# Optimization experiments

Hardware: AMD Instinct MI355X
Metric: run time of the kernel (lower is better)

Reference implementation:

```python
import jax, jax.numpy as jnp
import numpy as np

N = 50000      # nodes
E = 400000     # edges
D = 128        # embedding_depth
H = 4          # attention heads
DK = 32        # per-head dim (graph_message_depth / heads)
NR = 50        # num_radial
L = 2          # num_graph_convolutions
NG = 100       # graphs in batch
NT = 100       # atom type vocab
TE = 32        # atom_type_embedding_dims
OUT = 512      # bottleneck_dim
CUT = 6.0      # convolution_cutoff


def setup_inputs() -> dict:
    key = jax.random.key(0)
    ks = jax.random.split(key, 20)
    s = 0.05
    inp = {
        'pos': jax.random.normal(ks[0], (N, 3), jnp.float32) * 5.0,
        'atom_types': jax.random.randint(ks[1], (N,), 0, NT),
        'edge_index': jax.random.randint(ks[2], (2, E), 0, N),
        'batch': jnp.sort(jax.random.randint(ks[3], (N,), 0, NG)),
        'emb_table': jax.random.normal(ks[4], (NT, TE), jnp.float32) * s,
        'W_init': jax.random.normal(ks[5], (TE + 3, D), jnp.float32) * s,
        'b_init': jnp.zeros((D,), jnp.float32),
        'Wq': jax.random.normal(ks[6], (L, D, H * DK), jnp.float32) * s,
        'Wk': jax.random.normal(ks[7], (L, D, H * DK), jnp.float32) * s,
        'Wv': jax.random.normal(ks[8], (L, D, H * DK), jnp.float32) * s,
        'We': jax.random.normal(ks[9], (L, NR, H * DK), jnp.float32) * s,
        'Wo': jax.random.normal(ks[10], (L, H * DK, D), jnp.float32) * s,
        'Wm1': jax.random.normal(ks[11], (L, D, D), jnp.float32) * s,
        'bm1': jnp.zeros((L, D), jnp.float32),
        'Wm2': jax.random.normal(ks[12], (L, D, D), jnp.float32) * s,
        'bm2': jnp.zeros((L, D), jnp.float32),
        'ln_g': jnp.ones((L, D), jnp.float32),
        'ln_b': jnp.zeros((L, D), jnp.float32),
        'W_out': jax.random.normal(ks[13], (D, OUT), jnp.float32) * s,
        'b_out': jnp.zeros((OUT,), jnp.float32),
    }
    return inp


def _layernorm(x, g, b):
    m = jnp.mean(x, -1, keepdims=True)
    v = jnp.var(x, -1, keepdims=True)
    return (x - m) * jax.lax.rsqrt(v + 1e-5) * g + b


def _rbf(d):
    # Gaussian radial basis with smooth cosine cutoff envelope
    mus = jnp.linspace(0.0, CUT, NR)
    gamma = (NR / CUT) ** 2
    env = 0.5 * (jnp.cos(jnp.pi * jnp.minimum(d, CUT) / CUT) + 1.0)
    return jnp.exp(-gamma * (d[:, None] - mus[None, :]) ** 2) * env[:, None]


def _seg_softmax(logits, seg, n):
    # logits: [E, H], segmented softmax over incoming edges per node
    m = jax.ops.segment_max(logits, seg, num_segments=n)
    e = jnp.exp(logits - m[seg])
    s = jax.ops.segment_sum(e, seg, num_segments=n)
    return e / (s[seg] + 1e-9)


def _forward(pos, atom_types, edge_index, batch, emb_table, W_init, b_init,
             Wq, Wk, Wv, We, Wo, Wm1, bm1, Wm2, bm2, ln_g, ln_b, W_out, b_out):
    src, dst = edge_index[0], edge_index[1]
    # atom type embedding + concat positions -> init node features
    x0 = jnp.concatenate([emb_table[atom_types], pos], axis=-1)  # [N, TE+3]
    x = x0 @ W_init + b_init                                     # [N, D]
    # radial features per edge
    d = jnp.linalg.norm(pos[src] - pos[dst] + 1e-8, axis=-1)     # [E]
    rb = _rbf(d)                                                 # [E, NR]
    scale = 1.0 / jnp.sqrt(jnp.float32(DK))
    for l in range(L):
        qn, kn, vn = x @ Wq[l], x @ Wk[l], x @ Wv[l]             # [N, H*DK]
        q = qn[dst].reshape(E, H, DK)
        k = kn[src].reshape(E, H, DK)
        v = vn[src].reshape(E, H, DK)
        e = (rb @ We[l]).reshape(E, H, DK)
        logits = jnp.sum(q * (k + e), axis=-1) * scale           # [E, H]
        a = _seg_softmax(logits, dst, N)                         # [E, H]
        msg = jax.ops.segment_sum(a[..., None] * (v + e), dst, num_segments=N)
        x = x + msg.reshape(N, H * DK) @ Wo[l]
        # nodewise FC block with pre-norm and residual
        h = _layernorm(x, ln_g[l], ln_b[l])
        h = jax.nn.gelu(h @ Wm1[l] + bm1[l])
        x = x + h @ Wm2[l] + bm2[l]
    # sum graph aggregation, then output projection to bottleneck
    g = jax.ops.segment_sum(x, batch, num_segments=NG)           # [NG, D]
    return g @ W_out + b_out                                     # [NG, OUT]


def reference(pos, atom_types, edge_index, batch, emb_table, W_init, b_init,
              Wq, Wk, Wv, We, Wo, Wm1, bm1, Wm2, bm2, ln_g, ln_b, W_out, b_out):
    return _forward(pos, atom_types, edge_index, batch, emb_table, W_init, b_init,
                    Wq, Wk, Wv, We, Wo, Wm1, bm1, Wm2, bm2, ln_g, ln_b, W_out, b_out)
```

## Files before the change

kernel.cpp:

```cpp
#include <hip/hip_runtime.h>
#include <math.h>

#define NN 50000
#define NE 400000
#define DDIM 128
#define NHEAD 4
#define NRAD 50
#define NGRAPH 100
#define NTYPE 100
#define TEMB 32
#define DOUT 512
#define CUTF 6.0f
#define PI_F 3.14159265358979323846f

#define SCAN_N ((NN + 255) / 256)

typedef unsigned int uint;
typedef unsigned short ushort;
typedef __attribute__((ext_vector_type(8))) short short8;
typedef __attribute__((ext_vector_type(4))) float f32x4;


__device__ __forceinline__ float gelu_tanh(float v) {
  float u = 0.7978845608028654f * (v + 0.044715f * v * v * v);
  return 0.5f * v * (1.0f + tanhf(u));
}

__device__ __forceinline__ ushort f2bf(float f) {
  uint u = __float_as_uint(f);
  uint r = (u + 0x7fffu + ((u >> 16) & 1u)) >> 16;
  return (ushort)r;
}
__device__ __forceinline__ float bfl(uint u) { return __uint_as_float(u << 16); }
__device__ __forceinline__ float bfh(uint u) { return __uint_as_float(u & 0xffff0000u); }

__device__ __forceinline__ float red16(float v) {
  v += __int_as_float(__builtin_amdgcn_update_dpp(0, __float_as_int(v), 0xB1, 0xF, 0xF, true));
  v += __int_as_float(__builtin_amdgcn_update_dpp(0, __float_as_int(v), 0x4E, 0xF, 0xF, true));
  v += __int_as_float(__builtin_amdgcn_update_dpp(0, __float_as_int(v), 0x141, 0xF, 0xF, true));
  v += __int_as_float(__builtin_amdgcn_update_dpp(0, __float_as_int(v), 0x140, 0xF, 0xF, true));
  return v;
}
__device__ __forceinline__ float red8(float v) {
  v += __int_as_float(__builtin_amdgcn_update_dpp(0, __float_as_int(v), 0xB1, 0xF, 0xF, true));
  v += __int_as_float(__builtin_amdgcn_update_dpp(0, __float_as_int(v), 0x4E, 0xF, 0xF, true));
  v += __int_as_float(__builtin_amdgcn_update_dpp(0, __float_as_int(v), 0x141, 0xF, 0xF, true));
  return v;
}

__global__ void k_fill_f(float* p, float v, int n) {
  int i = blockIdx.x * blockDim.x + threadIdx.x;
  if (i < n) p[i] = v;
}
__global__ void k_fill_i(int* p, int v, int n) {
  int i = blockIdx.x * blockDim.x + threadIdx.x;
  if (i < n) p[i] = v;
}


__global__ void k_wconv(const float* __restrict__ Wq, const float* __restrict__ Wk,
                        const float* __restrict__ Wv, const float* __restrict__ Wo,
                        const float* __restrict__ Wm1, const float* __restrict__ Wm2,
                        ushort* __restrict__ Wtb) {
  int idx = blockIdx.x * 256 + threadIdx.x;
  int m = idx >> 14;
  int r = idx & 16383;
  int c = r >> 7, k = r & 127;
  int l = m / 6, fam = m % 6;
  const float* src = fam == 0 ? Wq : fam == 1 ? Wk : fam == 2 ? Wv
                   : fam == 3 ? Wo : fam == 4 ? Wm1 : Wm2;
  Wtb[idx] = f2bf(src[l * 16384 + k * 128 + c]);
}


__global__ void k_wewo(const float* __restrict__ We, const float* __restrict__ Wo,
                       ushort* __restrict__ WW) {
  int idx = blockIdx.x * 256 + threadIdx.x;
  int l = idx >> 15;
  int r = idx & 32767;
  int c = r >> 8, k = r & 255;
  float acc = 0.f;
  if (k < 200) {
    int j = k >> 2, h = k & 3;
    const float* we = We + (size_t)l * NRAD * DDIM + j * DDIM + 32 * h;
    const float* wo = Wo + (size_t)l * DDIM * DDIM + (size_t)(32 * h) * DDIM + c;
#pragma unroll 8
    for (int dk = 0; dk < 32; ++dk) acc = fmaf(we[dk], wo[(size_t)dk * DDIM], acc);
  }
  WW[idx] = f2bf(acc);
}


__global__ void k_wqe(const float* __restrict__ Wq, const float* __restrict__ We,
                      ushort* __restrict__ WQET) {
  int idx = blockIdx.x * 256 + threadIdx.x;
  int l = idx >> 15;
  int r = idx & 32767;
  int col = r >> 7, d = r & 127;
  float acc = 0.f;
  if (col < 200) {
    int j = col >> 2, h = col & 3;
    const float* wq = Wq + (size_t)l * 16384 + (size_t)d * 128 + 32 * h;
    const float* we = We + (size_t)l * NRAD * DDIM + j * DDIM + 32 * h;
#pragma unroll 8
    for (int u = 0; u < 32; ++u) acc = fmaf(wq[u], we[u], acc);
  }
  WQET[idx] = f2bf(acc);
}


__global__ void k_embw(const float* __restrict__ emb, const float* __restrict__ W,
                       const float* __restrict__ b, float* __restrict__ embW) {
  int idx = blockIdx.x * 256 + threadIdx.x;
  if (idx >= NTYPE * DDIM) return;
  int a = idx >> 7, c = idx & 127;
  const float* er = emb + (size_t)a * TEMB;
  float acc = b[c];
#pragma unroll
  for (int t = 0; t < TEMB; ++t) acc = fmaf(er[t], W[t * DDIM + c], acc);
  embW[idx] = acc;
}


__global__ void k_init2(const float* __restrict__ pos, const int* __restrict__ at,
                        const float* __restrict__ embW, const float* __restrict__ W,
                        float* __restrict__ x) {
  int idx = blockIdx.x * blockDim.x + threadIdx.x;
  if (idx >= NN * 32) return;
  int n = idx >> 5, c4 = (idx & 31) << 2;
  float4 e = *(const float4*)&embW[(size_t)at[n] * DDIM + c4];
  float px = pos[n * 3 + 0], py = pos[n * 3 + 1], pz = pos[n * 3 + 2];
  float4 wx = *(const float4*)&W[(TEMB + 0) * DDIM + c4];
  float4 wy = *(const float4*)&W[(TEMB + 1) * DDIM + c4];
  float4 wz = *(const float4*)&W[(TEMB + 2) * DDIM + c4];
  float4 o;
  o.x = e.x + px * wx.x + py * wy.x + pz * wz.x;
  o.y = e.y + px * wx.y + py * wy.y + pz * wz.y;
  o.z = e.z + px * wx.z + py * wy.z + pz * wz.z;
  o.w = e.w + px * wx.w + py * wy.w + pz * wz.w;
  *(float4*)&x[(size_t)n * DDIM + c4] = o;
}


__global__ void k_edge(const float* __restrict__ pos, const int* __restrict__ ei,
                       float* __restrict__ de, int* __restrict__ deg) {
  int e = blockIdx.x * blockDim.x + threadIdx.x;
  if (e >= NE) return;
  int s = ei[e], t = ei[NE + e];
  float dx = pos[s * 3 + 0] - pos[t * 3 + 0] + 1e-8f;
  float dy = pos[s * 3 + 1] - pos[t * 3 + 1] + 1e-8f;
  float dz = pos[s * 3 + 2] - pos[t * 3 + 2] + 1e-8f;
  de[e] = sqrtf(dx * dx + dy * dy + dz * dz);
  atomicAdd(&deg[t], 1);
}


__global__ void k_scan1(const int* __restrict__ deg, int* __restrict__ bsum) {
  __shared__ int red[256];
  int i = blockIdx.x * 256 + threadIdx.x;
  red[threadIdx.x] = (i < NN) ? deg[i] : 0;
  __syncthreads();
  for (int off = 128; off > 0; off >>= 1) {
    if (threadIdx.x < off) red[threadIdx.x] += red[threadIdx.x + off];
    __syncthreads();
  }
  if (threadIdx.x == 0) bsum[blockIdx.x] = red[0];
}

__global__ void k_scan2(int* __restrict__ bsum) {
  __shared__ int sh[256];
  int t = threadIdx.x;
  int v = (t < SCAN_N) ? bsum[t] : 0;
  sh[t] = v;
  __syncthreads();
  for (int off = 1; off < 256; off <<= 1) {
    int u = (t >= off) ? sh[t - off] : 0;
    __syncthreads();
    sh[t] += u;
    __syncthreads();
  }
  if (t < SCAN_N) bsum[t] = (t == 0) ? 0 : sh[t - 1];
}

__global__ void k_scan3(const int* __restrict__ deg, const int* __restrict__ bsum,
                        int* __restrict__ rowptr, int* __restrict__ cnear,
                        int* __restrict__ cfar) {
  __shared__ int sh[256];
  int t = threadIdx.x;
  int i = blockIdx.x * 256 + t;
  int v = (i < NN) ? deg[i] : 0;
  sh[t] = v;
  __syncthreads();
  for (int off = 1; off < 256; off <<= 1) {
    int u = (t >= off) ? sh[t - off] : 0;
    __syncthreads();
    sh[t] += u;
    __syncthreads();
  }
  int excl = bsum[blockIdx.x] + sh[t] - v;
  if (i < NN) {
    rowptr[i] = excl;
    cnear[i] = excl;
    cfar[i] = excl + v;
    if (i == NN - 1) rowptr[NN] = excl + v;
  }
}

__global__ void k_scatter(const int* __restrict__ ei, const float* __restrict__ de,
                          int* __restrict__ cnear, int* __restrict__ cfar,
                          int2* __restrict__ er) {
  int e = blockIdx.x * blockDim.x + threadIdx.x;
  if (e >= NE) return;
  int src = ei[e], dst = ei[NE + e];
  float d = de[e];
  int idx;
  if (d < CUTF)
    idx = atomicAdd(&cnear[dst], 1);
  else
    idx = atomicSub(&cfar[dst], 1) - 1;
  er[idx] = make_int2(src, __float_as_int(d));
}


__global__ __launch_bounds__(256) void k_qkv(
    const float* __restrict__ x, const ushort* __restrict__ Wt3,
    const ushort* __restrict__ WQET, ushort* __restrict__ qo,
    ushort* __restrict__ ko, ushort* __restrict__ vo, ushort* __restrict__ qe) {
  __shared__ ushort Al[128 * 128];
  __shared__ ushort Wl[128 * 128];
  const int tid = threadIdx.x;
  const int r0 = blockIdx.x * 128;

  for (int i = tid; i < 128 * 16; i += 256) {
    int r = i >> 4, g = i & 15;
    int gr = r0 + r;
    float4 f0 = {0, 0, 0, 0}, f1 = {0, 0, 0, 0};
    if (gr < NN) {
      f0 = *(const float4*)&x[(size_t)gr * 128 + g * 8];
      f1 = *(const float4*)&x[(size_t)gr * 128 + g * 8 + 4];
    }
    int gs = g ^ (r & 7);
    ushort4 u0 = {f2bf(f0.x), f2bf(f0.y), f2bf(f0.z), f2bf(f0.w)};
    ushort4 u1 = {f2bf(f1.x), f2bf(f1.y), f2bf(f1.z), f2bf(f1.w)};
    *(ushort4*)&Al[r * 128 + gs * 8] = u0;
    *(ushort4*)&Al[r * 128 + gs * 8 + 4] = u1;
  }

  const int w = tid >> 6, l = tid & 63;
  const int lg = l >> 4, lr = l & 15;

  for (int m = 0; m < 5; ++m) {
    const ushort* wsrc = (m < 3) ? (Wt3 + m * 16384) : (WQET + (m - 3) * 16384);
    for (int i = tid; i < 128 * 16; i += 256) {
      int c = i >> 4, g = i & 15;
      ushort4 w0 = *(const ushort4*)&wsrc[c * 128 + g * 8];
      ushort4 w1 = *(const ushort4*)&wsrc[c * 128 + g * 8 + 4];
      int gs = g ^ (c & 7);
      *(ushort4*)&Wl[c * 128 + gs * 8] = w0;
      *(ushort4*)&Wl[c * 128 + gs * 8 + 4] = w1;
    }
    __syncthreads();

    f32x4 acc[2][8];
#pragma unroll
    for (int rt = 0; rt < 2; ++rt)
#pragma unroll
      for (int ct = 0; ct < 8; ++ct) acc[rt][ct] = (f32x4){0.f, 0.f, 0.f, 0.f};

#pragma unroll
    for (int ks = 0; ks < 4; ++ks) {
      short8 af[2];
#pragma unroll
      for (int rt = 0; rt < 2; ++rt) {
        int arow = w * 32 + rt * 16 + lr;
        int ga = (ks * 4 + lg) ^ (arow & 7);
        af[rt] = *(const short8*)&Al[arow * 128 + ga * 8];
      }
#pragma unroll
      for (int ct = 0; ct < 8; ++ct) {
        int col = ct * 16 + lr;
        int gb = (ks * 4 + lg) ^ (col & 7);
        short8 bf = *(const short8*)&Wl[col * 128 + gb * 8];
#pragma unroll
        for (int rt = 0; rt < 2; ++rt)
          acc[rt][ct] = __builtin_amdgcn_mfma_f32_16x16x32_bf16(af[rt], bf, acc[rt][ct], 0, 0, 0);
      }
    }

    if (m < 3) {
      ushort* o = (m == 0) ? qo : (m == 1) ? ko : vo;
#pragma unroll
      for (int rt = 0; rt < 2; ++rt)
#pragma unroll
        for (int ct = 0; ct < 8; ++ct) {
          int col = ct * 16 + lr;
#pragma unroll
          for (int r = 0; r < 4; ++r) {
            int row = r0 + w * 32 + rt * 16 + lg * 4 + r;
            if (row < NN) o[(size_t)row * 128 + col] = f2bf(acc[rt][ct][r]);
          }
        }
    } else {
      int cb = (m - 3) * 128;
#pragma unroll
      for (int rt = 0; rt < 2; ++rt)
#pragma unroll
        for (int ct = 0; ct < 8; ++ct) {
          int col = cb + ct * 16 + lr;
          if (col < 200) {
#pragma unroll
            for (int r = 0; r < 4; ++r) {
              int row = r0 + w * 32 + rt * 16 + lg * 4 + r;
              if (row < NN) qe[(size_t)row * 200 + col] = f2bf(acc[rt][ct][r]);
            }
          }
        }
    }
    __syncthreads();
  }
}


template <bool BIAS, bool GELU, bool RESID, bool LNF, bool EXTK>
__global__ __launch_bounds__(256) void k_gemm2(
    const ushort* __restrict__ A, const ushort* __restrict__ Wt,
    const float* __restrict__ bias, const float* __restrict__ resid,
    void* __restrict__ outp, const float* __restrict__ lng,
    const float* __restrict__ lnb, ushort* __restrict__ lnout,
    const ushort* __restrict__ arbn, const ushort* __restrict__ WW) {
  __shared__ ushort Al[128 * 128];
  __shared__ ushort Wl[128 * 128];
  const int tid = threadIdx.x;
  const int r0 = blockIdx.x * 128;

  for (int i = tid; i < 128 * 16; i += 256) {
    int r = i >> 4, g = i & 15;
    int gr = r0 + r;
    ushort4 v0 = {0, 0, 0, 0}, v1 = {0, 0, 0, 0};
    if (gr < NN) {
      v0 = *(const ushort4*)&A[(size_t)gr * 128 + g * 8];
      v1 = *(const ushort4*)&A[(size_t)gr * 128 + g * 8 + 4];
    }
    int gs = g ^ (r & 7);
    *(ushort4*)&Al[r * 128 + gs * 8] = v0;
    *(ushort4*)&Al[r * 128 + gs * 8 + 4] = v1;
  }
  for (int i = tid; i < 128 * 16; i += 256) {
    int c = i >> 4, g = i & 15;
    ushort4 w0 = *(const ushort4*)&Wt[c * 128 + g * 8];
    ushort4 w1 = *(const ushort4*)&Wt[c * 128 + g * 8 + 4];
    int gs = g ^ (c & 7);
    *(ushort4*)&Wl[c * 128 + gs * 8] = w0;
    *(ushort4*)&Wl[c * 128 + gs * 8 + 4] = w1;
  }
  __syncthreads();

  const int w = tid >> 6, l = tid & 63;
  const int lg = l >> 4, lr = l & 15;
  f32x4 acc[2][8];
#pragma unroll
  for (int rt = 0; rt < 2; ++rt)
#pragma unroll
    for (int ct = 0; ct < 8; ++ct) acc[rt][ct] = (f32x4){0.f, 0.f, 0.f, 0.f};

#pragma unroll
  for (int ks = 0; ks < 4; ++ks) {
    short8 af[2];
#pragma unroll
    for (int rt = 0; rt < 2; ++rt) {
      int arow = w * 32 + rt * 16 + lr;
      int ga = (ks * 4 + lg) ^ (arow & 7);
      af[rt] = *(const short8*)&Al[arow * 128 + ga * 8];
    }
#pragma unroll
    for (int ct = 0; ct < 8; ++ct) {
      int col = ct * 16 + lr;
      int gb = (ks * 4 + lg) ^ (col & 7);
      short8 bf = *(const short8*)&Wl[col * 128 + gb * 8];
#pragma unroll
      for (int rt = 0; rt < 2; ++rt)
        acc[rt][ct] = __builtin_amdgcn_mfma_f32_16x16x32_bf16(af[rt], bf, acc[rt][ct], 0, 0, 0);
    }
  }

  if (EXTK) {
    for (int q = 0; q < 2; ++q) {
      __syncthreads();
      for (int i = tid; i < 128 * 16; i += 256) {
        int r = i >> 4, g = i & 15;
        int gr = r0 + r;
        ushort4 v0 = {0, 0, 0, 0}, v1 = {0, 0, 0, 0};
        if (gr < NN && (q == 0 || g < 9)) {
          v0 = *(const ushort4*)&arbn[(size_t)gr * 200 + q * 128 + g * 8];
          v1 = *(const ushort4*)&arbn[(size_t)gr * 200 + q * 128 + g * 8 + 4];
        }
        int gs = g ^ (r & 7);
        *(ushort4*)&Al[r * 128 + gs * 8] = v0;
        *(ushort4*)&Al[r * 128 + gs * 8 + 4] = v1;
      }
      for (int i = tid; i < 128 * 16; i += 256) {
        int c = i >> 4, g = i & 15;
        ushort4 w0 = *(const ushort4*)&WW[c * 256 + q * 128 + g * 8];
        ushort4 w1 = *(const ushort4*)&WW[c * 256 + q * 128 + g * 8 + 4];
        int gs = g ^ (c & 7);
        *(ushort4*)&Wl[c * 128 + gs * 8] = w0;
        *(ushort4*)&Wl[c * 128 + gs * 8 + 4] = w1;
      }
      __syncthreads();
#pragma unroll
      for (int ks = 0; ks < 4; ++ks) {
        short8 af[2];
#pragma unroll
        for (int rt = 0; rt < 2; ++rt) {
          int arow = w * 32 + rt * 16 + lr;
          int ga = (ks * 4 + lg) ^ (arow & 7);
          af[rt] = *(const short8*)&Al[arow * 128 + ga * 8];
        }
#pragma unroll
        for (int ct = 0; ct < 8; ++ct) {
          int col = ct * 16 + lr;
          int gb = (ks * 4 + lg) ^ (col & 7);
          short8 bf = *(const short8*)&Wl[col * 128 + gb * 8];
#pragma unroll
          for (int rt = 0; rt < 2; ++rt)
            acc[rt][ct] = __builtin_amdgcn_mfma_f32_16x16x32_bf16(af[rt], bf, acc[rt][ct], 0, 0, 0);
        }
      }
    }
  }

#pragma unroll
  for (int rt = 0; rt < 2; ++rt)
#pragma unroll
    for (int r = 0; r < 4; ++r) {
      int row = r0 + w * 32 + rt * 16 + lg * 4 + r;
      bool ok = row < NN;
      float v[8];
#pragma unroll
      for (int ct = 0; ct < 8; ++ct) {
        int col = ct * 16 + lr;
        float vv = acc[rt][ct][r];
        if (BIAS) vv += bias[col];
        if (GELU) vv = gelu_tanh(vv);
        if (RESID) vv += ok ? resid[(size_t)row * 128 + col] : 0.f;
        v[ct] = vv;
      }
      if (RESID || LNF) {
        if (ok)
#pragma unroll
          for (int ct = 0; ct < 8; ++ct)
            ((float*)outp)[(size_t)row * 128 + ct * 16 + lr] = v[ct];
      } else {
        if (ok)
#pragma unroll
          for (int ct = 0; ct < 8; ++ct)
            ((ushort*)outp)[(size_t)row * 128 + ct * 16 + lr] = f2bf(v[ct]);
      }
      if (LNF) {
        float s = 0.f, ss = 0.f;
#pragma unroll
        for (int ct = 0; ct < 8; ++ct) {
          s += v[ct];
          ss = fmaf(v[ct], v[ct], ss);
        }
#pragma unroll
        for (int msk = 8; msk >= 1; msk >>= 1) {
          s += __shfl_xor(s, msk);
          ss += __shfl_xor(ss, msk);
        }
        float mean = s * (1.0f / DDIM);
        float var = ss * (1.0f / DDIM) - mean * mean;
        float inv = rsqrtf(var + 1e-5f);
        if (ok)
#pragma unroll
          for (int ct = 0; ct < 8; ++ct) {
            int col = ct * 16 + lr;
            lnout[(size_t)row * 128 + col] =
                f2bf((v[ct] - mean) * inv * lng[col] + lnb[col]);
          }
      }
    }
}


__device__ __forceinline__ float rbf_fill(float d, int j) {
  const float step = CUTF / (NRAD - 1);
  const float gamma = (NRAD / CUTF) * (NRAD / CUTF);
  float mu = j * step;
  float dm = d - mu;
  float env = 0.5f * (__cosf(PI_F * d / CUTF) + 1.0f);
  return __expf(-gamma * dm * dm) * env;
}

#define SCALE_QK 0.17677669529663687f

__global__ __launch_bounds__(256) void k_attn7(
    const ushort* __restrict__ qnb, const ushort* __restrict__ knb,
    const ushort* __restrict__ vnb, ushort* __restrict__ qe,
    const int2* __restrict__ er, const int* __restrict__ rowptr,
    const int* __restrict__ nearend, ushort* __restrict__ msgb) {
  __shared__ float qel[4][64][4];
  __shared__ float rbl[4][64];
  __shared__ float aml[4][128];
  const int tid = threadIdx.x;

  const int w = tid >> 6, t = tid & 63;
  const int n = blockIdx.x * 4 + w;
  const int h = t >> 4;
  const int j0 = t & 15;
  const int hw = t >> 5;
  const int c = t & 31;
  uint qu = *(const uint*)&qnb[(size_t)n * DDIM + 2 * t];
  const float q0 = bfl(qu), q1 = bfh(qu);
  uint2 qp = *(const uint2*)&qnb[(size_t)n * DDIM + 4 * c];
  const float fq0 = bfl(qp.x), fq1 = bfh(qp.x), fq2 = bfl(qp.y), fq3 = bfh(qp.y);
  if (t < NRAD) {
    ushort4 qv = *(const ushort4*)&qe[(size_t)n * 200 + 4 * t];
    qel[w][t][0] = bfl(qv.x);
    qel[w][t][1] = bfl(qv.y);
    qel[w][t][2] = bfl(qv.z);
    qel[w][t][3] = bfl(qv.w);
  } else {
    qel[w][t][0] = 0.f; qel[w][t][1] = 0.f; qel[w][t][2] = 0.f; qel[w][t][3] = 0.f;
  }
  const int start = rowptr[n], nend = nearend[n], end = rowptr[n + 1];

  float s = 0.f, a0 = 0.f, a1 = 0.f;
  float4 arb = {0.f, 0.f, 0.f, 0.f};

  for (int cb = start; cb < nend; cb += 64) {
    int cnt = min(nend - cb, 64);
    int2 e_t = make_int2(0, 0);
    if (t < cnt) e_t = er[cb + t];
    for (int i = 0; i < cnt; ++i) {
      int src = __shfl(e_t.x, i);
      float dd = __shfl(__int_as_float(e_t.y), i);
      uint ku = *(const uint*)&knb[(size_t)src * DDIM + 2 * t];
      uint vu = *(const uint*)&vnb[(size_t)src * DDIM + 2 * t];
      float pr = q0 * bfl(ku) + q1 * bfh(ku);
      float rb = (t < NRAD) ? rbf_fill(dd, t) : 0.f;
      rbl[w][t] = rb;
      pr = fmaf(rbl[w][j0], qel[w][j0][h], pr);
      pr = fmaf(rbl[w][j0 + 16], qel[w][j0 + 16][h], pr);
      pr = fmaf(rbl[w][j0 + 32], qel[w][j0 + 32][h], pr);
      pr = fmaf(rbl[w][j0 + 48], qel[w][j0 + 48][h], pr);
      pr = red16(pr);
      float ae = __expf(fminf(pr * SCALE_QK, 60.f));
      s += ae;
      a0 = fmaf(ae, bfl(vu), a0);
      a1 = fmaf(ae, bfh(vu), a1);
      float aex = __shfl(ae, 0);
      float aey = __shfl(ae, 16);
      float aez = __shfl(ae, 32);
      float aew = __shfl(ae, 48);
      arb.x = fmaf(rb, aex, arb.x);
      arb.y = fmaf(rb, aey, arb.y);
      arb.z = fmaf(rb, aez, arb.z);
      arb.w = fmaf(rb, aew, arb.w);
    }
  }

  float sf = 0.f, af0 = 0.f, af1 = 0.f, af2 = 0.f, af3 = 0.f;
  for (int cb = nend; cb < end; cb += 64) {
    int cnt = min(end - cb, 64);
    int src_t = 0;
    if (t < cnt) src_t = er[cb + t].x;
    for (int i = hw; i < cnt; i += 2) {
      int src = __shfl(src_t, i);
      uint2 ku = *(const uint2*)&knb[(size_t)src * DDIM + 4 * c];
      uint2 vu = *(const uint2*)&vnb[(size_t)src * DDIM + 4 * c];
      float pr = fq0 * bfl(ku.x) + fq1 * bfh(ku.x);
      pr = fmaf(fq2, bfl(ku.y), pr);
      pr = fmaf(fq3, bfh(ku.y), pr);
      pr = red8(pr);
      float ae = __expf(fminf(pr * SCALE_QK, 60.f));
      sf += ae;
      af0 = fmaf(ae, bfl(vu.x), af0);
      af1 = fmaf(ae, bfh(vu.x), af1);
      af2 = fmaf(ae, bfl(vu.y), af2);
      af3 = fmaf(ae, bfh(vu.y), af3);
    }
  }
  sf += __shfl_xor(sf, 32);
  af0 += __shfl_xor(af0, 32);
  af1 += __shfl_xor(af1, 32);
  af2 += __shfl_xor(af2, 32);
  af3 += __shfl_xor(af3, 32);
  aml[w][4 * c + 0] = af0;
  aml[w][4 * c + 1] = af1;
  aml[w][4 * c + 2] = af2;
  aml[w][4 * c + 3] = af3;
  a0 += aml[w][2 * t];
  a1 += aml[w][2 * t + 1];

  float4 s4;
  s4.x = __shfl(s, 0) + __shfl(sf, 0);
  s4.y = __shfl(s, 16) + __shfl(sf, 8);
  s4.z = __shfl(s, 32) + __shfl(sf, 16);
  s4.w = __shfl(s, 48) + __shfl(sf, 24);
  float4 inv4 = {1.f / (s4.x + 1e-9f), 1.f / (s4.y + 1e-9f),
                 1.f / (s4.z + 1e-9f), 1.f / (s4.w + 1e-9f)};
  float invo = (h == 0) ? inv4.x : (h == 1) ? inv4.y : (h == 2) ? inv4.z : inv4.w;
  if (t < NRAD) {
    ushort4 o = {f2bf(arb.x * inv4.x), f2bf(arb.y * inv4.y),
                 f2bf(arb.z * inv4.z), f2bf(arb.w * inv4.w)};
    *(ushort4*)&qe[(size_t)n * 200 + 4 * t] = o;
  }
  a0 *= invo;
  a1 *= invo;
  uint pk = (uint)f2bf(a0) | ((uint)f2bf(a1) << 16);
  *(uint*)&msgb[(size_t)n * DDIM + 2 * t] = pk;
}


#define GS_NODES 32
__global__ void k_graphsum(const float* __restrict__ x, const int* __restrict__ batch,
                           float* __restrict__ g) {
  int t = threadIdx.x;
  int n0 = blockIdx.x * GS_NODES;
  int nend = n0 + GS_NODES;
  if (nend > NN) nend = NN;
  if (n0 >= NN) return;
  float acc = 0.f;
  int cur = batch[n0];
  for (int n = n0; n < nend; ++n) {
    int bb = batch[n];
    if (bb != cur) {
      atomicAdd(&g[(size_t)cur * DDIM + t], acc);
      acc = 0.f;
      cur = bb;
    }
    acc += x[(size_t)n * DDIM + t];
  }
  atomicAdd(&g[(size_t)cur * DDIM + t], acc);
}


__global__ void k_out(const float* __restrict__ g, const float* __restrict__ W,
                      const float* __restrict__ b, float* __restrict__ out) {
  int idx = blockIdx.x * blockDim.x + threadIdx.x;
  if (idx >= NGRAPH * DOUT) return;
  int r = idx / DOUT, c = idx % DOUT;
  float acc = b[c];
#pragma unroll 8
  for (int k = 0; k < DDIM; ++k) acc = fmaf(g[r * DDIM + k], W[k * DOUT + c], acc);
  out[idx] = acc;
}


extern "C" void kernel_launch(void* const* d_in, const int* in_sizes, int n_in,
                              void* d_out, int out_size, void* d_ws, size_t ws_size,
                              hipStream_t stream) {
  const float* pos = (const float*)d_in[0];
  const int* at = (const int*)d_in[1];
  const int* ei = (const int*)d_in[2];
  const int* batch = (const int*)d_in[3];
  const float* emb = (const float*)d_in[4];
  const float* W_init = (const float*)d_in[5];
  const float* b_init = (const float*)d_in[6];
  const float* Wq = (const float*)d_in[7];
  const float* Wk = (const float*)d_in[8];
  const float* Wv = (const float*)d_in[9];
  const float* We = (const float*)d_in[10];
  const float* Wo = (const float*)d_in[11];
  const float* Wm1 = (const float*)d_in[12];
  const float* bm1 = (const float*)d_in[13];
  const float* Wm2 = (const float*)d_in[14];
  const float* bm2 = (const float*)d_in[15];
  const float* ln_g = (const float*)d_in[16];
  const float* ln_b = (const float*)d_in[17];
  const float* W_out = (const float*)d_in[18];
  const float* b_out = (const float*)d_in[19];
  float* out = (float*)d_out;

  const size_t ND = (size_t)NN * DDIM;
  float* x = (float*)d_ws;
  ushort* qnb = (ushort*)(x + ND);
  ushort* knb = qnb + ND;
  ushort* vnb = knb + ND;
  ushort* msgb = vnb + ND;
  ushort* qe = msgb + ND;
  ushort* Wtb = qe + (size_t)NN * 200;
  ushort* WW = Wtb + 12 * 16384;
  ushort* WQET = WW + 2 * 32768;
  float* embW = (float*)(WQET + 2 * 32768);
  float* de = embW + NTYPE * DDIM;
  int* deg = (int*)(de + NE);
  int* cnear = deg + NN;
  int* cfar = cnear + NN;
  int* rowptr = cfar + NN;
  int2* er = (int2*)(rowptr + NN + 64);
  float* gb = (float*)(er + NE);
  int* bsum = (int*)(gb + NGRAPH * DDIM);

  ushort* hb = qnb;
  ushort* h2 = knb;

  k_wconv<<<12 * 16384 / 256, 256, 0, stream>>>(Wq, Wk, Wv, Wo, Wm1, Wm2, Wtb);
  k_wewo<<<2 * 32768 / 256, 256, 0, stream>>>(We, Wo, WW);
  k_wqe<<<2 * 32768 / 256, 256, 0, stream>>>(Wq, We, WQET);
  k_embw<<<(NTYPE * DDIM + 255) / 256, 256, 0, stream>>>(emb, W_init, b_init, embW);
  k_fill_i<<<(NN + 255) / 256, 256, 0, stream>>>(deg, 0, NN);
  k_init2<<<(NN * 32 + 255) / 256, 256, 0, stream>>>(pos, at, embW, W_init, x);
  k_edge<<<(NE + 255) / 256, 256, 0, stream>>>(pos, ei, de, deg);
  k_scan1<<<SCAN_N, 256, 0, stream>>>(deg, bsum);
  k_scan2<<<1, 256, 0, stream>>>(bsum);
  k_scan3<<<SCAN_N, 256, 0, stream>>>(deg, bsum, rowptr, cnear, cfar);
  k_scatter<<<(NE + 255) / 256, 256, 0, stream>>>(ei, de, cnear, cfar, er);

  const int gg = (NN + 127) / 128;
  for (int l = 0; l < 2; ++l) {
    const ushort* Wt_l = Wtb + (size_t)l * 6 * 16384;
    const ushort* WQET_l = WQET + (size_t)l * 32768;
    const ushort* WW_l = WW + (size_t)l * 32768;

    k_qkv<<<gg, 256, 0, stream>>>(x, Wt_l, WQET_l, qnb, knb, vnb, qe);
    k_attn7<<<NN / 4, 256, 0, stream>>>(qnb, knb, vnb, qe, er, rowptr, cnear, msgb);

    k_gemm2<false, false, true, true, true><<<gg, 256, 0, stream>>>(
        msgb, Wt_l + 3 * 16384, nullptr, x, x,
        ln_g + (size_t)l * DDIM, ln_b + (size_t)l * DDIM, hb, qe, WW_l);
    k_gemm2<true, true, false, false, false><<<gg, 256, 0, stream>>>(
        hb, Wt_l + 4 * 16384, bm1 + (size_t)l * DDIM, nullptr, h2,
        nullptr, nullptr, nullptr, nullptr, nullptr);
    k_gemm2<true, false, true, false, false><<<gg, 256, 0, stream>>>(
        h2, Wt_l + 5 * 16384, bm2 + (size_t)l * DDIM, x, x,
        nullptr, nullptr, nullptr, nullptr, nullptr);
  }

  k_fill_f<<<(NGRAPH * DDIM + 255) / 256, 256, 0, stream>>>(gb, 0.f, NGRAPH * DDIM);
  k_graphsum<<<(NN + GS_NODES - 1) / GS_NODES, 128, 0, stream>>>(x, batch, gb);
  k_out<<<(NGRAPH * DOUT + 255) / 256, 256, 0, stream>>>(gb, W_out, b_out, out);
}
```

Measured before the change: 357.3 us.

## Interleave K and V rows into one buffer and merge setup kernels

K and V projections are now written interleaved per element into a single 256-wide bf16 row buffer. The attention kernel can then fetch each neighbour's K and V values with one wider load instead of two separate gathers. Five small preprocessing kernels are also merged into one block-partitioned kernel to cut launch count. The interleaved stores from the QKV GEMM are strided, which may make its write-out less coalesced.

```diff
diff --git a/kernel.cpp b/kernel.cpp
--- a/kernel.cpp
+++ b/kernel.cpp
@@ -52,73 +52,68 @@
   int i = blockIdx.x * blockDim.x + threadIdx.x;
   if (i < n) p[i] = v;
 }
-__global__ void k_fill_i(int* p, int v, int n) {
-  int i = blockIdx.x * blockDim.x + threadIdx.x;
-  if (i < n) p[i] = v;
-}
-
-
-__global__ void k_wconv(const float* __restrict__ Wq, const float* __restrict__ Wk,
-                        const float* __restrict__ Wv, const float* __restrict__ Wo,
-                        const float* __restrict__ Wm1, const float* __restrict__ Wm2,
-                        ushort* __restrict__ Wtb) {
-  int idx = blockIdx.x * 256 + threadIdx.x;
-  int m = idx >> 14;
-  int r = idx & 16383;
-  int c = r >> 7, k = r & 127;
-  int l = m / 6, fam = m % 6;
-  const float* src = fam == 0 ? Wq : fam == 1 ? Wk : fam == 2 ? Wv
-                   : fam == 3 ? Wo : fam == 4 ? Wm1 : Wm2;
-  Wtb[idx] = f2bf(src[l * 16384 + k * 128 + c]);
-}
-
-
-__global__ void k_wewo(const float* __restrict__ We, const float* __restrict__ Wo,
-                       ushort* __restrict__ WW) {
-  int idx = blockIdx.x * 256 + threadIdx.x;
-  int l = idx >> 15;
-  int r = idx & 32767;
-  int c = r >> 8, k = r & 255;
-  float acc = 0.f;
-  if (k < 200) {
-    int j = k >> 2, h = k & 3;
-    const float* we = We + (size_t)l * NRAD * DDIM + j * DDIM + 32 * h;
-    const float* wo = Wo + (size_t)l * DDIM * DDIM + (size_t)(32 * h) * DDIM + c;
+
+
+__global__ void k_pre(const float* __restrict__ Wq, const float* __restrict__ Wk,
+                      const float* __restrict__ Wv, const float* __restrict__ Wo,
+                      const float* __restrict__ Wm1, const float* __restrict__ Wm2,
+                      const float* __restrict__ We, const float* __restrict__ emb,
+                      const float* __restrict__ Wi, const float* __restrict__ bi,
+                      ushort* __restrict__ Wtb, ushort* __restrict__ WW,
+                      ushort* __restrict__ WQET, float* __restrict__ embW,
+                      int* __restrict__ deg) {
+  int b = blockIdx.x;
+  if (b < 768) {
+    int idx = b * 256 + threadIdx.x;
+    int m = idx >> 14;
+    int r = idx & 16383;
+    int c = r >> 7, k = r & 127;
+    int l = m / 6, fam = m % 6;
+    const float* src = fam == 0 ? Wq : fam == 1 ? Wk : fam == 2 ? Wv
+                     : fam == 3 ? Wo : fam == 4 ? Wm1 : Wm2;
+    Wtb[idx] = f2bf(src[l * 16384 + k * 128 + c]);
+  } else if (b < 1024) {
+    int idx = (b - 768) * 256 + threadIdx.x;
+    int l = idx >> 15;
+    int r = idx & 32767;
+    int c = r >> 8, k = r & 255;
+    float acc = 0.f;
+    if (k < 200) {
+      int j = k >> 2, h = k & 3;
+      const float* we = We + (size_t)l * NRAD * DDIM + j * DDIM + 32 * h;
+      const float* wo = Wo + (size_t)l * DDIM * DDIM + (size_t)(32 * h) * DDIM + c;
 #pragma unroll 8
-    for (int dk = 0; dk < 32; ++dk) acc = fmaf(we[dk], wo[(size_t)dk * DDIM], acc);
-  }
-  WW[idx] = f2bf(acc);
-}
-
-
-__global__ void k_wqe(const float* __restrict__ Wq, const float* __restrict__ We,
-                      ushort* __restrict__ WQET) {
-  int idx = blockIdx.x * 256 + threadIdx.x;
-  int l = idx >> 15;
-  int r = idx & 32767;
-  int col = r >> 7, d = r & 127;
-  float acc = 0.f;
-  if (col < 200) {
-    int j = col >> 2, h = col & 3;
-    const float* wq = Wq + (size_t)l * 16384 + (size_t)d * 128 + 32 * h;
-    const float* we = We + (size_t)l * NRAD * DDIM + j * DDIM + 32 * h;
+      for (int dk = 0; dk < 32; ++dk) acc = fmaf(we[dk], wo[(size_t)dk * DDIM], acc);
+    }
+    WW[idx] = f2bf(acc);
+  } else if (b < 1280) {
+    int idx = (b - 1024) * 256 + threadIdx.x;
+    int l = idx >> 15;
+    int r = idx & 32767;
+    int col = r >> 7, d = r & 127;
+    float acc = 0.f;
+    if (col < 200) {
+      int j = col >> 2, h = col & 3;
+      const float* wq = Wq + (size_t)l * 16384 + (size_t)d * 128 + 32 * h;
+      const float* we = We + (size_t)l * NRAD * DDIM + j * DDIM + 32 * h;
 #pragma unroll 8
-    for (int u = 0; u < 32; ++u) acc = fmaf(wq[u], we[u], acc);
-  }
-  WQET[idx] = f2bf(acc);
-}
-
-
-__global__ void k_embw(const float* __restrict__ emb, const float* __restrict__ W,
-                       const float* __restrict__ b, float* __restrict__ embW) {
-  int idx = blockIdx.x * 256 + threadIdx.x;
-  if (idx >= NTYPE * DDIM) return;
-  int a = idx >> 7, c = idx & 127;
-  const float* er = emb + (size_t)a * TEMB;
-  float acc = b[c];
-#pragma unroll
-  for (int t = 0; t < TEMB; ++t) acc = fmaf(er[t], W[t * DDIM + c], acc);
-  embW[idx] = acc;
+      for (int u = 0; u < 32; ++u) acc = fmaf(wq[u], we[u], acc);
+    }
+    WQET[idx] = f2bf(acc);
+  } else if (b < 1330) {
+    int idx = (b - 1280) * 256 + threadIdx.x;
+    if (idx < NTYPE * DDIM) {
+      int a = idx >> 7, c = idx & 127;
+      const float* er = emb + (size_t)a * TEMB;
+      float acc = bi[c];
+#pragma unroll
+      for (int t = 0; t < TEMB; ++t) acc = fmaf(er[t], Wi[t * DDIM + c], acc);
+      embW[idx] = acc;
+    }
+  } else {
+    int idx = (b - 1330) * 256 + threadIdx.x;
+    if (idx < NN) deg[idx] = 0;
+  }
 }
 
 
@@ -225,7 +220,7 @@
 __global__ __launch_bounds__(256) void k_qkv(
     const float* __restrict__ x, const ushort* __restrict__ Wt3,
     const ushort* __restrict__ WQET, ushort* __restrict__ qo,
-    ushort* __restrict__ ko, ushort* __restrict__ vo, ushort* __restrict__ qe) {
+    ushort* __restrict__ kvb, ushort* __restrict__ qe) {
   __shared__ ushort Al[128 * 128];
   __shared__ ushort Wl[128 * 128];
   const int tid = threadIdx.x;
@@ -287,8 +282,7 @@
       }
     }
 
-    if (m < 3) {
-      ushort* o = (m == 0) ? qo : (m == 1) ? ko : vo;
+    if (m == 0) {
 #pragma unroll
       for (int rt = 0; rt < 2; ++rt)
 #pragma unroll
@@ -297,7 +291,20 @@
 #pragma unroll
           for (int r = 0; r < 4; ++r) {
             int row = r0 + w * 32 + rt * 16 + lg * 4 + r;
-            if (row < NN) o[(size_t)row * 128 + col] = f2bf(acc[rt][ct][r]);
+            if (row < NN) qo[(size_t)row * 128 + col] = f2bf(acc[rt][ct][r]);
+          }
+        }
+    } else if (m < 3) {
+      int off = m - 1;
+#pragma unroll
+      for (int rt = 0; rt < 2; ++rt)
+#pragma unroll
+        for (int ct = 0; ct < 8; ++ct) {
+          int col = ct * 16 + lr;
+#pragma unroll
+          for (int r = 0; r < 4; ++r) {
+            int row = r0 + w * 32 + rt * 16 + lg * 4 + r;
+            if (row < NN) kvb[(size_t)row * 256 + 2 * col + off] = f2bf(acc[rt][ct][r]);
           }
         }
     } else {
@@ -494,11 +501,11 @@
 
 #define SCALE_QK 0.17677669529663687f
 
-__global__ __launch_bounds__(256) void k_attn7(
-    const ushort* __restrict__ qnb, const ushort* __restrict__ knb,
-    const ushort* __restrict__ vnb, ushort* __restrict__ qe,
-    const int2* __restrict__ er, const int* __restrict__ rowptr,
-    const int* __restrict__ nearend, ushort* __restrict__ msgb) {
+__global__ __launch_bounds__(256) void k_attn8(
+    const ushort* __restrict__ qnb, const ushort* __restrict__ kvb,
+    ushort* __restrict__ qe, const int2* __restrict__ er,
+    const int* __restrict__ rowptr, const int* __restrict__ nearend,
+    ushort* __restrict__ msgb) {
   __shared__ float qel[4][64][4];
   __shared__ float rbl[4][64];
   __shared__ float aml[4][128];
@@ -535,9 +542,8 @@
     for (int i = 0; i < cnt; ++i) {
       int src = __shfl(e_t.x, i);
       float dd = __shfl(__int_as_float(e_t.y), i);
-      uint ku = *(const uint*)&knb[(size_t)src * DDIM + 2 * t];
-      uint vu = *(const uint*)&vnb[(size_t)src * DDIM + 2 * t];
-      float pr = q0 * bfl(ku) + q1 * bfh(ku);
+      uint2 kv = *(const uint2*)&kvb[(size_t)src * 256 + 4 * t];
+      float pr = q0 * bfl(kv.x) + q1 * bfl(kv.y);
       float rb = (t < NRAD) ? rbf_fill(dd, t) : 0.f;
       rbl[w][t] = rb;
       pr = fmaf(rbl[w][j0], qel[w][j0][h], pr);
@@ -547,8 +553,8 @@
       pr = red16(pr);
       float ae = __expf(fminf(pr * SCALE_QK, 60.f));
       s += ae;
-      a0 = fmaf(ae, bfl(vu), a0);
-      a1 = fmaf(ae, bfh(vu), a1);
+      a0 = fmaf(ae, bfh(kv.x), a0);
+      a1 = fmaf(ae, bfh(kv.y), a1);
       float aex = __shfl(ae, 0);
       float aey = __shfl(ae, 16);
       float aez = __shfl(ae, 32);
@@ -567,18 +573,17 @@
     if (t < cnt) src_t = er[cb + t].x;
     for (int i = hw; i < cnt; i += 2) {
       int src = __shfl(src_t, i);
-      uint2 ku = *(const uint2*)&knb[(size_t)src * DDIM + 4 * c];
-      uint2 vu = *(const uint2*)&vnb[(size_t)src * DDIM + 4 * c];
-      float pr = fq0 * bfl(ku.x) + fq1 * bfh(ku.x);
-      pr = fmaf(fq2, bfl(ku.y), pr);
-      pr = fmaf(fq3, bfh(ku.y), pr);
+      uint4 kv = *(const uint4*)&kvb[(size_t)src * 256 + 8 * c];
+      float pr = fq0 * bfl(kv.x) + fq1 * bfl(kv.y);
+      pr = fmaf(fq2, bfl(kv.z), pr);
+      pr = fmaf(fq3, bfl(kv.w), pr);
       pr = red8(pr);
       float ae = __expf(fminf(pr * SCALE_QK, 60.f));
       sf += ae;
-      af0 = fmaf(ae, bfl(vu.x), af0);
-      af1 = fmaf(ae, bfh(vu.x), af1);
-      af2 = fmaf(ae, bfl(vu.y), af2);
-      af3 = fmaf(ae, bfh(vu.y), af3);
+      af0 = fmaf(ae, bfh(kv.x), af0);
+      af1 = fmaf(ae, bfh(kv.y), af1);
+      af2 = fmaf(ae, bfh(kv.z), af2);
+      af3 = fmaf(ae, bfh(kv.w), af3);
     }
   }
   sf += __shfl_xor(sf, 32);
@@ -676,9 +681,8 @@
   const size_t ND = (size_t)NN * DDIM;
   float* x = (float*)d_ws;
   ushort* qnb = (ushort*)(x + ND);
-  ushort* knb = qnb + ND;
-  ushort* vnb = knb + ND;
-  ushort* msgb = vnb + ND;
+  ushort* kvb = qnb + ND;
+  ushort* msgb = kvb + 2 * ND;
   ushort* qe = msgb + ND;
   ushort* Wtb = qe + (size_t)NN * 200;
   ushort* WW = Wtb + 12 * 16384;
@@ -694,13 +698,10 @@
   int* bsum = (int*)(gb + NGRAPH * DDIM);
 
   ushort* hb = qnb;
-  ushort* h2 = knb;
-
-  k_wconv<<<12 * 16384 / 256, 256, 0, stream>>>(Wq, Wk, Wv, Wo, Wm1, Wm2, Wtb);
-  k_wewo<<<2 * 32768 / 256, 256, 0, stream>>>(We, Wo, WW);
-  k_wqe<<<2 * 32768 / 256, 256, 0, stream>>>(Wq, We, WQET);
-  k_embw<<<(NTYPE * DDIM + 255) / 256, 256, 0, stream>>>(emb, W_init, b_init, embW);
-  k_fill_i<<<(NN + 255) / 256, 256, 0, stream>>>(deg, 0, NN);
+  ushort* h2 = kvb;
+
+  k_pre<<<1526, 256, 0, stream>>>(Wq, Wk, Wv, Wo, Wm1, Wm2, We, emb, W_init, b_init,
+                                  Wtb, WW, WQET, embW, deg);
   k_init2<<<(NN * 32 + 255) / 256, 256, 0, stream>>>(pos, at, embW, W_init, x);
   k_edge<<<(NE + 255) / 256, 256, 0, stream>>>(pos, ei, de, deg);
   k_scan1<<<SCAN_N, 256, 0, stream>>>(deg, bsum);
@@ -714,8 +715,8 @@
     const ushort* WQET_l = WQET + (size_t)l * 32768;
     const ushort* WW_l = WW + (size_t)l * 32768;
 
-    k_qkv<<<gg, 256, 0, stream>>>(x, Wt_l, WQET_l, qnb, knb, vnb, qe);
-    k_attn7<<<NN / 4, 256, 0, stream>>>(qnb, knb, vnb, qe, er, rowptr, cnear, msgb);
+    k_qkv<<<gg, 256, 0, stream>>>(x, Wt_l, WQET_l, qnb, kvb, qe);
+    k_attn8<<<NN / 4, 256, 0, stream>>>(qnb, kvb, qe, er, rowptr, cnear, msgb);
 
     k_gemm2<false, false, true, true, true><<<gg, 256, 0, stream>>>(
         msgb, Wt_l + 3 * 16384, nullptr, x, x,
```

Result: no change. 352.4 us (-1.4%).
